# Kernel optimization log

Measured on AMD Instinct MI355X. Metric: run time of the kernel, lower is better.

## Reference

```python
import jax, jax.numpy as jnp
import numpy as np

C, D, K15, K16, OUT = 64, 8, 15, 16, 512
B = 32768


def setup_inputs() -> dict:
    key = jax.random.key(0)
    kx, kS, kH, kT, kL = jax.random.split(key, 5)
    x = jax.random.normal(kx, (B, C * D), dtype=jnp.float32)
    S = jax.random.normal(kS, (C, D, K15), dtype=jnp.float32)
    H = jax.random.normal(kH, (K15, K16), dtype=jnp.float32)
    T = jax.random.normal(kT, (C, K15), dtype=jnp.float32)
    LUT = jax.random.normal(kL, (C, K16, OUT), dtype=jnp.float32)
    return {"x": x, "S": S, "H": H, "T": T, "LUT": LUT}


def reference(x, S, H, T, LUT):
    b = x.shape[0]
    xv = x.reshape(b, C, D)                              # (B, C, D)
    p = jnp.einsum('bcd,cdk->bck', xv, S) - T            # (B, C, 15)
    # torch sets zeros to -1 before sign => sign(x)==-1 when x<=0
    s = jnp.where(p > 0, jnp.float32(1.0), jnp.float32(-1.0))
    h = jnp.einsum('bck,kj->bcj', s, H)                  # (B, C, 16)
    idx = jnp.argmax(h, axis=-1)                         # (B, C) int
    # one_hot @ LUT == direct gather of LUT[c, idx[b,c], :]
    vals = LUT[jnp.arange(C)[None, :], idx]              # (B, C, OUT)
    return jnp.sum(vals, axis=1)                         # (B, OUT)
```

## Files before the change

kernel.cpp:

```cpp
#include <hip/hip_runtime.h>
#include <stdint.h>

#define B_    32768
#define C_    64
#define D_    8
#define K15_  15
#define K16_  16
#define OUT_  512

typedef _Float16 half4v __attribute__((ext_vector_type(4)));
typedef _Float16 half8  __attribute__((ext_vector_type(8)));

#define AMAP_OFF  0
#define AMAP_SZ   32768
#define S64_OFF   32768
#define S64_SZ    (64 * 15 * 8 * 8)
#define T64_OFF   (S64_OFF + S64_SZ)
#define T64_SZ    (64 * 15 * 8)
#define IDX_OFF   (T64_OFF + T64_SZ)
#define IDX_SZ    (B_ * C_)
#define S32_SZ    (64 * 15 * 8 * 4)
#define PCT_OFF   (IDX_OFF + IDX_SZ)
#define PCT_SZ    (B_ * 32)
#define PTAB_OFF  (PCT_OFF + PCT_SZ)
#define PTAB_SZ   (32 * 32 * 256 * 16 * 2)
#define WS_NEED   ((size_t)PTAB_OFF + PTAB_SZ)

__device__ __forceinline__ void gld_lds16(const void* g, void* l) {
    __builtin_amdgcn_global_load_lds(
        (const __attribute__((address_space(1))) void*)g,
        (__attribute__((address_space(3))) void*)l, 16, 0, 0);
}

__global__ __launch_bounds__(256) void k_setup(const float* __restrict__ LUT,
                                               const float* __restrict__ H,
                                               const float* __restrict__ S,
                                               const float* __restrict__ T,
                                               _Float16* __restrict__ P5,
                                               uint8_t* __restrict__ amap,
                                               double* __restrict__ S64,
                                               double* __restrict__ T64,
                                               float* __restrict__ S32,
                                               float* __restrict__ T32,
                                               int do_pairs) {
    int gid = blockIdx.x * 256 + threadIdx.x;

    if (do_pairs) {
        int e8 = gid & 1;
        int q = (gid >> 1) & 255;
        int jc = (gid >> 9) & 31;
        int p = gid >> 14;
        int t0 = q >> 4;
        int t1 = q & 15;
        int j0 = jc * 16 + e8 * 8;
        const float* u = LUT + (size_t)((2 * p) * 16 + t0) * 512 + j0;
        const float* v = LUT + (size_t)((2 * p + 1) * 16 + t1) * 512 + j0;
        float4 u0 = ((const float4*)u)[0];
        float4 u1 = ((const float4*)u)[1];
        float4 v0 = ((const float4*)v)[0];
        float4 v1 = ((const float4*)v)[1];
        half8 w;
        w[0] = (_Float16)(u0.x + v0.x);
        w[1] = (_Float16)(u0.y + v0.y);
        w[2] = (_Float16)(u0.z + v0.z);
        w[3] = (_Float16)(u0.w + v0.w);
        w[4] = (_Float16)(u1.x + v1.x);
        w[5] = (_Float16)(u1.y + v1.y);
        w[6] = (_Float16)(u1.z + v1.z);
        w[7] = (_Float16)(u1.w + v1.w);
        *(half8*)(P5 + (size_t)gid * 8) = w;
    }

    if (blockIdx.x < 128) {
        int code = gid;
        double h[K16_];
#pragma unroll
        for (int j = 0; j < K16_; ++j) h[j] = 0.0;
#pragma unroll
        for (int k = 0; k < K15_; ++k) {
            double s = ((code >> k) & 1) ? 1.0 : -1.0;
#pragma unroll
            for (int j = 0; j < K16_; ++j) h[j] += s * (double)H[k * K16_ + j];
        }
        double best = h[0];
        int bi = 0;
#pragma unroll
        for (int j = 1; j < K16_; ++j) {
            if (h[j] > best) { best = h[j]; bi = j; }
        }
        amap[code] = (uint8_t)bi;
    } else if (blockIdx.x == 128) {
        for (int i = threadIdx.x; i < 64 * 15 * 8; i += 256) {
            int c = i / 120;
            int r = i - c * 120;
            int k = r >> 3;
            int d = r & 7;
            float sv = S[c * 120 + d * 15 + k];
            S64[i] = (double)sv;
            if (do_pairs) S32[i] = sv;
        }
        for (int i = threadIdx.x; i < 64 * 15; i += 256) {
            T64[i] = (double)T[i];
            if (do_pairs) T32[i] = T[i];
        }
    }
}

#define XST2 587
#define CPAD 40
template <int FAST>
__global__ __launch_bounds__(256, 4) void k_codes4(const float* __restrict__ x,
                                                   const double* __restrict__ S64,
                                                   const double* __restrict__ T64,
                                                   const float* __restrict__ S32,
                                                   const float* __restrict__ T32,
                                                   const uint8_t* __restrict__ amap,
                                                   uint8_t* __restrict__ idxo,
                                                   uint8_t* __restrict__ pcT) {
    __shared__ float xls[8 * XST2];
    __shared__ alignas(16) uint16_t codesh[64 * CPAD];

    int bg = blockIdx.x >> 1;
    int hb = blockIdx.x & 1;
    int b0 = bg * 64;
    int lane = threadIdx.x & 63;
    int wv = __builtin_amdgcn_readfirstlane(threadIdx.x >> 6);

    for (int r = 0; r < 4; ++r) {
        __syncthreads();
#pragma unroll
        for (int t2 = 0; t2 < 4; ++t2) {
            int e = t2 * 256 + threadIdx.x;
            int b = e >> 4;
            int j4 = e & 15;
            float4 v = ((const float4*)(x + (size_t)(b0 + b) * 512 +
                                        hb * 256 + r * 64))[j4];
            int cl = j4 >> 1;
            int d0 = (j4 & 1) * 4;
            float* dst = &xls[cl * XST2 + b * 9 + d0];
            dst[0] = v.x; dst[1] = v.y; dst[2] = v.z; dst[3] = v.w;
        }
        __syncthreads();
#pragma unroll
        for (int i = 0; i < 2; ++i) {
            int cl = wv + i * 4;
            int c = hb * 32 + r * 8 + cl;
            unsigned code = 0;
            if (FAST) {
                const float* Sc = S32 + c * 120;
                const float* Tc = T32 + c * 15;
                float xf[8];
#pragma unroll
                for (int d = 0; d < 8; ++d)
                    xf[d] = xls[cl * XST2 + lane * 9 + d];
                float pmin = 3.0e38f;
#pragma unroll
                for (int k = 0; k < K15_; ++k) {
                    float p = -Tc[k];
#pragma unroll
                    for (int d = 0; d < 8; ++d)
                        p = fmaf(xf[d], Sc[k * 8 + d], p);
                    code |= (p > 0.f) ? (1u << k) : 0u;
                    pmin = fminf(pmin, fabsf(p));
                }
                if (pmin < 1e-4f) {
                    const double* Sd = S64 + c * 120;
                    const double* Td = T64 + c * 15;
                    code = 0;
#pragma unroll
                    for (int k = 0; k < K15_; ++k) {
                        double p = -Td[k];
#pragma unroll
                        for (int d = 0; d < 8; ++d)
                            p = fma((double)xf[d], Sd[k * 8 + d], p);
                        code |= (p > 0.0) ? (1u << k) : 0u;
                    }
                }
            } else {
                const double* Sc = S64 + c * 120;
                const double* Tc = T64 + c * 15;
                double xd[8];
#pragma unroll
                for (int d = 0; d < 8; ++d)
                    xd[d] = (double)xls[cl * XST2 + lane * 9 + d];
#pragma unroll
                for (int k = 0; k < K15_; ++k) {
                    double p = -Tc[k];
#pragma unroll
                    for (int d = 0; d < 8; ++d)
                        p = fma(xd[d], Sc[k * 8 + d], p);
                    code |= (p > 0.0) ? (1u << k) : 0u;
                }
            }
            codesh[lane * CPAD + r * 8 + cl] = (uint16_t)code;
        }
    }
    __syncthreads();

    int bb = threadIdx.x >> 2;
    int q = threadIdx.x & 3;
    uint4 cw4 = *(const uint4*)&codesh[bb * CPAD + q * 8];
    uint16_t cds[8];
    cds[0] = (uint16_t)(cw4.x & 0xFFFF); cds[1] = (uint16_t)(cw4.x >> 16);
    cds[2] = (uint16_t)(cw4.y & 0xFFFF); cds[3] = (uint16_t)(cw4.y >> 16);
    cds[4] = (uint16_t)(cw4.z & 0xFFFF); cds[5] = (uint16_t)(cw4.z >> 16);
    cds[6] = (uint16_t)(cw4.w & 0xFFFF); cds[7] = (uint16_t)(cw4.w >> 16);
    uint8_t ids[8];
#pragma unroll
    for (int j = 0; j < 8; ++j) ids[j] = amap[cds[j]];

    if (FAST) {
        int row = b0 + bb;
        int rg = row >> 10;
        int tr = row & 127;
        int i_ = (row & 1023) >> 7;
        uint8_t* base = pcT + rg * 1024 + tr * 8 + i_;
#pragma unroll
        for (int j = 0; j < 4; ++j) {
            int p = hb * 16 + q * 4 + j;
            base[p * 32768] = (uint8_t)((ids[2 * j] << 4) | ids[2 * j + 1]);
        }
    } else {
        uint32_t w0 = (uint32_t)ids[0] | ((uint32_t)ids[1] << 8) |
                      ((uint32_t)ids[2] << 16) | ((uint32_t)ids[3] << 24);
        uint32_t w1 = (uint32_t)ids[4] | ((uint32_t)ids[5] << 8) |
                      ((uint32_t)ids[6] << 16) | ((uint32_t)ids[7] << 24);
        uint32_t* o =
            (uint32_t*)(idxo + (size_t)(b0 + bb) * 64 + hb * 32 + q * 8);
        o[0] = w0; o[1] = w1;
    }
}

__global__ __launch_bounds__(256, 8) void k_main8(const uint8_t* __restrict__ pcT,
                                                  const _Float16* __restrict__ P5,
                                                  float* __restrict__ out) {
    __shared__ alignas(16) _Float16 slab[2][256 * 16];

    int rg5 = blockIdx.x >> 5;
    int jc = blockIdx.x & 31;
    int t = threadIdx.x;
    int tc = t & 1;
    int tr = t >> 1;
    int lane = t & 63;
    int wv = __builtin_amdgcn_readfirstlane(t >> 6);

    const uint8_t* cbase = pcT + (rg5 >> 1) * 1024 + tr * 8 + (rg5 & 1) * 4;

    float acc[4][8];
#pragma unroll
    for (int i = 0; i < 4; ++i)
#pragma unroll
        for (int e = 0; e < 8; ++e) acc[i][e] = 0.f;

    int hoff = wv * 512 + lane * 8;

    {
        const _Float16* g = P5 + (size_t)jc * 4096 + hoff;
        gld_lds16(g, &slab[0][wv * 512]);
        gld_lds16(g + 2048, &slab[0][wv * 512 + 2048]);
    }
    uint32_t cw = *(const uint32_t*)cbase;
    uint32_t cwn = 0;

    for (int p = 0; p < 32; ++p) {
        __syncthreads();

        if (p < 31) {
            const _Float16* g =
                P5 + (size_t)((p + 1) * 32 + jc) * 4096 + hoff;
            _Float16* d = &slab[(p + 1) & 1][wv * 512];
            gld_lds16(g, d);
            gld_lds16(g + 2048, d + 2048);
            cwn = *(const uint32_t*)(cbase + (size_t)(p + 1) * 32768);
        }

        const _Float16* rb = &slab[p & 1][0] + tc * 8;
        uint32_t cw_cur = cw;
#pragma unroll
        for (int i = 0; i < 4; ++i) {
            int ci = (int)((cw_cur >> (8 * i)) & 0xFF);
            half8 v = *(const half8*)(rb + ci * 16);
#pragma unroll
            for (int e = 0; e < 8; ++e)
                acc[i][e] = fmaf((float)v[e], 1.0f, acc[i][e]);
        }
        cw = cwn;
    }

#pragma unroll
    for (int i = 0; i < 4; ++i) {
        int row = rg5 * 512 + i * 128 + tr;
        float* o = out + (size_t)row * 512 + jc * 16 + tc * 8;
        float4 w0;
        w0.x = acc[i][0]; w0.y = acc[i][1]; w0.z = acc[i][2]; w0.w = acc[i][3];
        float4 w1;
        w1.x = acc[i][4]; w1.y = acc[i][5]; w1.z = acc[i][6]; w1.w = acc[i][7];
        ((float4*)o)[0] = w0;
        ((float4*)o)[1] = w1;
    }
}

__global__ __launch_bounds__(256) void k_main_direct(const uint8_t* __restrict__ idx,
                                                     const float* __restrict__ LUT,
                                                     float* __restrict__ out) {
    int j4 = threadIdx.x & 127;
    int sub = threadIdx.x >> 7;
    int b0 = blockIdx.x * 16 + sub * 8;
    const float4* L4 = (const float4*)LUT;
    for (int r = 0; r < 8; ++r) {
        int b = b0 + r;
        const uint32_t* iw = (const uint32_t*)(idx + (size_t)b * 64);
        float4 acc;
        acc.x = 0.f; acc.y = 0.f; acc.z = 0.f; acc.w = 0.f;
#pragma unroll
        for (int i = 0; i < 16; ++i) {
            uint32_t w = __builtin_amdgcn_readfirstlane(iw[i]);
#pragma unroll
            for (int t = 0; t < 4; ++t) {
                int c = i * 4 + t;
                uint32_t codev = (w >> (8 * t)) & 0xFu;
                float4 v = L4[(size_t)(c * 16 + codev) * 128 + j4];
                acc.x += v.x; acc.y += v.y; acc.z += v.z; acc.w += v.w;
            }
        }
        ((float4*)(out + (size_t)b * 512))[j4] = acc;
    }
}

extern "C" void kernel_launch(void* const* d_in, const int* in_sizes, int n_in,
                              void* d_out, int out_size, void* d_ws, size_t ws_size,
                              hipStream_t stream) {
    const float* x   = (const float*)d_in[0];
    const float* S   = (const float*)d_in[1];
    const float* H   = (const float*)d_in[2];
    const float* T   = (const float*)d_in[3];
    const float* LUT = (const float*)d_in[4];
    float* out = (float*)d_out;

    uint8_t* ws = (uint8_t*)d_ws;
    uint8_t* amap = ws + AMAP_OFF;
    double* S64   = (double*)(ws + S64_OFF);
    double* T64   = (double*)(ws + T64_OFF);
    uint8_t* idxb = ws + IDX_OFF;
    float* S32    = (float*)(ws + IDX_OFF);
    float* T32    = (float*)(ws + IDX_OFF + S32_SZ);
    uint8_t* pcTb = ws + PCT_OFF;
    _Float16* P5  = (_Float16*)(ws + PTAB_OFF);

    bool use_pairs = ws_size >= WS_NEED;

    hipLaunchKernelGGL(k_setup, dim3(use_pairs ? 2048 : 129), dim3(256), 0,
                       stream, LUT, H, S, T, P5, amap, S64, T64, S32, T32,
                       use_pairs ? 1 : 0);
    if (use_pairs) {
        hipLaunchKernelGGL((k_codes4<1>), dim3(B_ / 64 * 2), dim3(256), 0,
                           stream, x, S64, T64, S32, T32, amap, idxb, pcTb);
        hipLaunchKernelGGL(k_main8, dim3(2048), dim3(256), 0, stream,
                           pcTb, P5, out);
    } else {
        hipLaunchKernelGGL((k_codes4<0>), dim3(B_ / 64 * 2), dim3(256), 0,
                           stream, x, S64, T64, S32, T32, amap, idxb, pcTb);
        hipLaunchKernelGGL(k_main_direct, dim3(B_ / 16), dim3(256), 0, stream,
                           idxb, LUT, out);
    }
}
```

Measured before the change: 174.4 us.

## Split code kernel into quarter-channel blocks with register-prefetched x and fma_mix accumulation

The code-computation kernel now gives each block a quarter of the channels (16) instead of half, which doubles the grid and raises the occupancy hint. The next x tile is prefetched into registers while the first 8 channels are being processed, so the global load overlaps compute. The main accumulation kernel replaces explicit half-to-float conversion plus FMA with inline v_fma_mix_f32 asm that reads the fp16 halves directly. The costs are more blocks each doing less work, more register pressure from the prefetch buffers, and reliance on inline asm.

```diff
diff --git a/kernel.cpp b/kernel.cpp
--- a/kernel.cpp
+++ b/kernel.cpp
@@ -10,6 +10,7 @@
 
 typedef _Float16 half4v __attribute__((ext_vector_type(4)));
 typedef _Float16 half8  __attribute__((ext_vector_type(8)));
+typedef uint32_t uint4v __attribute__((ext_vector_type(4)));
 
 #define AMAP_OFF  0
 #define AMAP_SZ   32768
@@ -30,6 +31,15 @@
     __builtin_amdgcn_global_load_lds(
         (const __attribute__((address_space(1))) void*)g,
         (__attribute__((address_space(3))) void*)l, 16, 0, 0);
+}
+
+__device__ __forceinline__ void fma_mix_lo(float& acc, uint32_t w, float one) {
+    asm("v_fma_mix_f32 %0, %1, %2, %0 op_sel_hi:[1,0,0]"
+        : "+v"(acc) : "v"(w), "v"(one));
+}
+__device__ __forceinline__ void fma_mix_hi(float& acc, uint32_t w, float one) {
+    asm("v_fma_mix_f32 %0, %1, %2, %0 op_sel:[1,0,0] op_sel_hi:[1,0,0]"
+        : "+v"(acc) : "v"(w), "v"(one));
 }
 
 __global__ __launch_bounds__(256) void k_setup(const float* __restrict__ LUT,
@@ -106,10 +116,10 @@
     }
 }
 
-#define XST2 587
-#define CPAD 40
+#define XST3 579
+#define CPAD2 24
 template <int FAST>
-__global__ __launch_bounds__(256, 4) void k_codes4(const float* __restrict__ x,
+__global__ __launch_bounds__(256, 6) void k_codes5(const float* __restrict__ x,
                                                    const double* __restrict__ S64,
                                                    const double* __restrict__ T64,
                                                    const float* __restrict__ S32,
@@ -117,34 +127,53 @@
                                                    const uint8_t* __restrict__ amap,
                                                    uint8_t* __restrict__ idxo,
                                                    uint8_t* __restrict__ pcT) {
-    __shared__ float xls[8 * XST2];
-    __shared__ alignas(16) uint16_t codesh[64 * CPAD];
-
-    int bg = blockIdx.x >> 1;
-    int hb = blockIdx.x & 1;
+    __shared__ float xls[8 * XST3];
+    __shared__ alignas(16) uint16_t codesh[64 * CPAD2];
+
+    int bg = blockIdx.x >> 2;
+    int cq = blockIdx.x & 3;
     int b0 = bg * 64;
     int lane = threadIdx.x & 63;
     int wv = __builtin_amdgcn_readfirstlane(threadIdx.x >> 6);
-
-    for (int r = 0; r < 4; ++r) {
-        __syncthreads();
-#pragma unroll
-        for (int t2 = 0; t2 < 4; ++t2) {
-            int e = t2 * 256 + threadIdx.x;
-            int b = e >> 4;
-            int j4 = e & 15;
-            float4 v = ((const float4*)(x + (size_t)(b0 + b) * 512 +
-                                        hb * 256 + r * 64))[j4];
-            int cl = j4 >> 1;
-            int d0 = (j4 & 1) * 4;
-            float* dst = &xls[cl * XST2 + b * 9 + d0];
-            dst[0] = v.x; dst[1] = v.y; dst[2] = v.z; dst[3] = v.w;
-        }
-        __syncthreads();
+    int tid = threadIdx.x;
+
+    float4 rgA[4], rgB[4];
+#pragma unroll
+    for (int t2 = 0; t2 < 4; ++t2) {
+        int e = t2 * 256 + tid;
+        int b = e >> 4;
+        int j4 = e & 15;
+        rgA[t2] = *(const float4*)(x + (size_t)(b0 + b) * 512 + cq * 128 +
+                                   0 * 64 + j4 * 4);
+    }
+#pragma unroll
+    for (int t2 = 0; t2 < 4; ++t2) {
+        int e = t2 * 256 + tid;
+        int b = e >> 4;
+        int j4 = e & 15;
+        int cl = j4 >> 1;
+        int d0 = (j4 & 1) * 4;
+        float* dst = &xls[cl * XST3 + b * 9 + d0];
+        dst[0] = rgA[t2].x; dst[1] = rgA[t2].y;
+        dst[2] = rgA[t2].z; dst[3] = rgA[t2].w;
+    }
+    __syncthreads();
+
+#pragma unroll
+    for (int t2 = 0; t2 < 4; ++t2) {
+        int e = t2 * 256 + tid;
+        int b = e >> 4;
+        int j4 = e & 15;
+        rgB[t2] = *(const float4*)(x + (size_t)(b0 + b) * 512 + cq * 128 +
+                                   1 * 64 + j4 * 4);
+    }
+
+#pragma unroll
+    for (int r = 0; r < 2; ++r) {
 #pragma unroll
         for (int i = 0; i < 2; ++i) {
             int cl = wv + i * 4;
-            int c = hb * 32 + r * 8 + cl;
+            int c = cq * 16 + r * 8 + cl;
             unsigned code = 0;
             if (FAST) {
                 const float* Sc = S32 + c * 120;
@@ -152,7 +181,7 @@
                 float xf[8];
 #pragma unroll
                 for (int d = 0; d < 8; ++d)
-                    xf[d] = xls[cl * XST2 + lane * 9 + d];
+                    xf[d] = xls[cl * XST3 + lane * 9 + d];
                 float pmin = 3.0e38f;
 #pragma unroll
                 for (int k = 0; k < K15_; ++k) {
@@ -182,7 +211,7 @@
                 double xd[8];
 #pragma unroll
                 for (int d = 0; d < 8; ++d)
-                    xd[d] = (double)xls[cl * XST2 + lane * 9 + d];
+                    xd[d] = (double)xls[cl * XST3 + lane * 9 + d];
 #pragma unroll
                 for (int k = 0; k < K15_; ++k) {
                     double p = -Tc[k];
@@ -192,22 +221,37 @@
                     code |= (p > 0.0) ? (1u << k) : 0u;
                 }
             }
-            codesh[lane * CPAD + r * 8 + cl] = (uint16_t)code;
+            codesh[lane * CPAD2 + r * 8 + cl] = (uint16_t)code;
+        }
+        if (r == 0) {
+            __syncthreads();
+#pragma unroll
+            for (int t2 = 0; t2 < 4; ++t2) {
+                int e = t2 * 256 + tid;
+                int b = e >> 4;
+                int j4 = e & 15;
+                int cl = j4 >> 1;
+                int d0 = (j4 & 1) * 4;
+                float* dst = &xls[cl * XST3 + b * 9 + d0];
+                dst[0] = rgB[t2].x; dst[1] = rgB[t2].y;
+                dst[2] = rgB[t2].z; dst[3] = rgB[t2].w;
+            }
+            __syncthreads();
         }
     }
     __syncthreads();
 
-    int bb = threadIdx.x >> 2;
-    int q = threadIdx.x & 3;
-    uint4 cw4 = *(const uint4*)&codesh[bb * CPAD + q * 8];
-    uint16_t cds[8];
-    cds[0] = (uint16_t)(cw4.x & 0xFFFF); cds[1] = (uint16_t)(cw4.x >> 16);
-    cds[2] = (uint16_t)(cw4.y & 0xFFFF); cds[3] = (uint16_t)(cw4.y >> 16);
-    cds[4] = (uint16_t)(cw4.z & 0xFFFF); cds[5] = (uint16_t)(cw4.z >> 16);
-    cds[6] = (uint16_t)(cw4.w & 0xFFFF); cds[7] = (uint16_t)(cw4.w >> 16);
-    uint8_t ids[8];
-#pragma unroll
-    for (int j = 0; j < 8; ++j) ids[j] = amap[cds[j]];
+    int bb = tid >> 2;
+    int sub = tid & 3;
+    uint64_t cw8 = *(const uint64_t*)&codesh[bb * CPAD2 + sub * 4];
+    uint16_t cds[4];
+    cds[0] = (uint16_t)(cw8 & 0xFFFF);
+    cds[1] = (uint16_t)((cw8 >> 16) & 0xFFFF);
+    cds[2] = (uint16_t)((cw8 >> 32) & 0xFFFF);
+    cds[3] = (uint16_t)(cw8 >> 48);
+    uint8_t ids[4];
+#pragma unroll
+    for (int j = 0; j < 4; ++j) ids[j] = amap[cds[j]];
 
     if (FAST) {
         int row = b0 + bb;
@@ -215,23 +259,17 @@
         int tr = row & 127;
         int i_ = (row & 1023) >> 7;
         uint8_t* base = pcT + rg * 1024 + tr * 8 + i_;
-#pragma unroll
-        for (int j = 0; j < 4; ++j) {
-            int p = hb * 16 + q * 4 + j;
-            base[p * 32768] = (uint8_t)((ids[2 * j] << 4) | ids[2 * j + 1]);
-        }
+        int p0 = cq * 8 + sub * 2;
+        base[(size_t)p0 * 32768] = (uint8_t)((ids[0] << 4) | ids[1]);
+        base[(size_t)(p0 + 1) * 32768] = (uint8_t)((ids[2] << 4) | ids[3]);
     } else {
         uint32_t w0 = (uint32_t)ids[0] | ((uint32_t)ids[1] << 8) |
                       ((uint32_t)ids[2] << 16) | ((uint32_t)ids[3] << 24);
-        uint32_t w1 = (uint32_t)ids[4] | ((uint32_t)ids[5] << 8) |
-                      ((uint32_t)ids[6] << 16) | ((uint32_t)ids[7] << 24);
-        uint32_t* o =
-            (uint32_t*)(idxo + (size_t)(b0 + bb) * 64 + hb * 32 + q * 8);
-        o[0] = w0; o[1] = w1;
-    }
-}
-
-__global__ __launch_bounds__(256, 8) void k_main8(const uint8_t* __restrict__ pcT,
+        *(uint32_t*)(idxo + (size_t)(b0 + bb) * 64 + cq * 16 + sub * 4) = w0;
+    }
+}
+
+__global__ __launch_bounds__(256, 8) void k_main9(const uint8_t* __restrict__ pcT,
                                                   const _Float16* __restrict__ P5,
                                                   float* __restrict__ out) {
     __shared__ alignas(16) _Float16 slab[2][256 * 16];
@@ -251,6 +289,7 @@
     for (int i = 0; i < 4; ++i)
 #pragma unroll
         for (int e = 0; e < 8; ++e) acc[i][e] = 0.f;
+    float one = 1.0f;
 
     int hoff = wv * 512 + lane * 8;
 
@@ -280,9 +319,12 @@
         for (int i = 0; i < 4; ++i) {
             int ci = (int)((cw_cur >> (8 * i)) & 0xFF);
             half8 v = *(const half8*)(rb + ci * 16);
-#pragma unroll
-            for (int e = 0; e < 8; ++e)
-                acc[i][e] = fmaf((float)v[e], 1.0f, acc[i][e]);
+            uint4v w = __builtin_bit_cast(uint4v, v);
+#pragma unroll
+            for (int e2 = 0; e2 < 4; ++e2) {
+                fma_mix_lo(acc[i][2 * e2], w[e2], one);
+                fma_mix_hi(acc[i][2 * e2 + 1], w[e2], one);
+            }
         }
         cw = cwn;
     }
@@ -353,12 +395,12 @@
                        stream, LUT, H, S, T, P5, amap, S64, T64, S32, T32,
                        use_pairs ? 1 : 0);
     if (use_pairs) {
-        hipLaunchKernelGGL((k_codes4<1>), dim3(B_ / 64 * 2), dim3(256), 0,
+        hipLaunchKernelGGL((k_codes5<1>), dim3(B_ / 64 * 4), dim3(256), 0,
                            stream, x, S64, T64, S32, T32, amap, idxb, pcTb);
-        hipLaunchKernelGGL(k_main8, dim3(2048), dim3(256), 0, stream,
+        hipLaunchKernelGGL(k_main9, dim3(2048), dim3(256), 0, stream,
                            pcTb, P5, out);
     } else {
-        hipLaunchKernelGGL((k_codes4<0>), dim3(B_ / 64 * 2), dim3(256), 0,
+        hipLaunchKernelGGL((k_codes5<0>), dim3(B_ / 64 * 4), dim3(256), 0,
                            stream, x, S64, T64, S32, T32, amap, idxb, pcTb);
         hipLaunchKernelGGL(k_main_direct, dim3(B_ / 16), dim3(256), 0, stream,
                            idxb, LUT, out);
```

Measured after the change: 165.7 us. 5.0% less time.
